# Kernel optimization log

Hardware: AMD Instinct MI355X
Metric: run time of the kernel (lower is better)

Reference implementation:

```python
import jax, jax.numpy as jnp
import numpy as np

IN_FEATURES = 4096
OUT_FEATURES = 4096
RANKS = (1, 16, 16, 1)
M_IN = 16   # in_core_features, 16**3 == 4096
M_OUT = 16  # out_core_features
ORDER = 3


def setup_inputs() -> dict:
    key = jax.random.key(0)
    k_x, k0, k1, k2, kb = jax.random.split(key, 5)
    s = 0.05
    x = jax.random.normal(k_x, (2, 1024, IN_FEATURES), dtype=jnp.float32)
    core0 = jax.random.normal(k0, (RANKS[0], M_IN, M_OUT, RANKS[1]), dtype=jnp.float32) * s
    core1 = jax.random.normal(k1, (RANKS[1], M_IN, M_OUT, RANKS[2]), dtype=jnp.float32) * s
    core2 = jax.random.normal(k2, (RANKS[2], M_IN, M_OUT, RANKS[3]), dtype=jnp.float32) * s
    bound = 1.0 / np.sqrt(IN_FEATURES)
    bias = jax.random.uniform(kb, (OUT_FEATURES,), dtype=jnp.float32,
                              minval=-bound, maxval=bound)
    return {"x": x, "core0": core0, "core1": core1, "core2": core2, "bias": bias}


def reference(x, core0, core1, core2, bias):
    lead_shape = x.shape[:-1]
    pad = M_IN ** ORDER - IN_FEATURES  # 0 here, kept for generality
    xf = x.reshape(-1, IN_FEATURES)
    if pad:
        xf = jnp.pad(xf, ((0, 0), (0, pad)))
    t = xf.reshape(-1, M_IN, M_IN, M_IN)                 # [b, i1, i2, i3]
    # TT core chain contraction (cores: [r_i, i, o, r_{i+1}])
    t = jnp.einsum('bijk,pixq->bjkxq', t, core0)          # sum i1, r0 -> [b, i2, i3, o1, r1]
    t = jnp.einsum('bjkxq,qjyr->bkxyr', t, core1)         # sum i2, r1 -> [b, i3, o1, o2, r2]
    t = jnp.einsum('bkxyr,rkzs->bxyzs', t, core2)         # sum i3, r2 -> [b, o1, o2, o3, 1]
    out = t.reshape(t.shape[0], -1)[:, :OUT_FEATURES]     # truncate padded output dims
    out = out.reshape(*lead_shape, OUT_FEATURES) + bias
    return out
```

## Files before the change

### kernel.cpp

```cpp
#include <hip/hip_runtime.h>
#include <hip/hip_bf16.h>

typedef unsigned short ushort_t;
typedef __attribute__((ext_vector_type(4))) float f32x4;
typedef __attribute__((ext_vector_type(8))) short bf16x8;
typedef __attribute__((ext_vector_type(8))) unsigned short u16x8;

#define M_DIM 2048
#define N_DIM 4096
#define K_DIM 4096
#define BM 256
#define BN 128
#define BK 64
#define NT (K_DIM / BK)

#define MFMA16(a, b, c) __builtin_amdgcn_mfma_f32_16x16x32_bf16((a), (b), (c), 0, 0, 0)

__device__ __forceinline__ unsigned short f2bf(float f) {
  unsigned int u = __float_as_uint(f);
  u += 0x7FFFu + ((u >> 16) & 1u);
  return (unsigned short)(u >> 16);
}

__device__ __forceinline__ void async16(void* l, const void* g) {
  __builtin_amdgcn_global_load_lds(
      (const __attribute__((address_space(1))) void*)g,
      (__attribute__((address_space(3))) void*)l,
      16, 0, 0);
}

__global__ void k_prep(const float* __restrict__ x, ushort_t* __restrict__ o,
                       const float* __restrict__ c0, const float* __restrict__ c1,
                       const float* __restrict__ c2, ushort_t* __restrict__ wt) {
  __shared__ float sc1[16 * 260];
  const int bid = blockIdx.x;
  const int tid = threadIdx.x;
  if (bid < 2048) {
    const int n4 = (M_DIM * K_DIM) / 4;
    for (int i = bid * 256 + tid; i < n4; i += 2048 * 256) {
      float4 v = ((const float4*)x)[i];
      ushort4 r;
      r.x = f2bf(v.x); r.y = f2bf(v.y); r.z = f2bf(v.z); r.w = f2bf(v.w);
      ((ushort4*)o)[i] = r;
    }
  } else {
    const int out = bid - 2048;
    const int o3 = out & 15;
    const int o2 = (out >> 4) & 15;
    const int o1 = out >> 8;

    {
      const int q  = tid >> 4;
      const int i2 = tid & 15;
      const float* src = c1 + q * 4096 + i2 * 256 + o2 * 16;
      float* dst = &sc1[i2 * 260 + q * 16];
      #pragma unroll
      for (int rr = 0; rr < 4; ++rr)
        *(float4*)(dst + rr * 4) = *(const float4*)(src + rr * 4);
    }
    __syncthreads();

    const int i2 = tid & 15;
    const int i1 = tid >> 4;

    float4 a4[4];
    {
      const float* c0p = c0 + (i1 * 16 + o1) * 16;
      #pragma unroll
      for (int rr = 0; rr < 4; ++rr) a4[rr] = *(const float4*)(c0p + rr * 4);
    }

    float t01r[16];
    #pragma unroll
    for (int r = 0; r < 16; ++r) t01r[r] = 0.f;
    #pragma unroll
    for (int q = 0; q < 16; ++q) {
      const float a = a4[q >> 2][q & 3];
      const float* sp = &sc1[i2 * 260 + q * 16];
      #pragma unroll
      for (int rr = 0; rr < 4; ++rr) {
        float4 v = *(const float4*)(sp + rr * 4);
        t01r[rr * 4 + 0] += a * v.x;
        t01r[rr * 4 + 1] += a * v.y;
        t01r[rr * 4 + 2] += a * v.z;
        t01r[rr * 4 + 3] += a * v.w;
      }
    }

    u16x8 lo, hi;
    #pragma unroll
    for (int i3 = 0; i3 < 16; ++i3) {
      const float* c2p = c2 + i3 * 16 + o3;
      float s = 0.f;
      #pragma unroll
      for (int rr = 0; rr < 16; ++rr) s += t01r[rr] * c2p[rr * 256];
      ushort_t v = f2bf(s);
      if (i3 < 8) lo[i3] = v; else hi[i3 - 8] = v;
    }
    u16x8* dst = (u16x8*)(wt + ((size_t)out << 12) + (i1 << 8) + (i2 << 4));
    dst[0] = lo;
    dst[1] = hi;
  }
}

__global__ __launch_bounds__(512, 2) void k_gemm(
    const ushort_t* __restrict__ A,
    const ushort_t* __restrict__ Bt,
    const float* __restrict__ bias,
    float* __restrict__ C)
{
  __shared__ ushort_t lA[3][BM * BK];
  __shared__ ushort_t lB[3][BN * BK];

  const int tid  = threadIdx.x;
  const int lane = tid & 63;
  const int wid  = tid >> 6;
  const int wm   = wid >> 1;
  const int wn   = wid & 1;
  const int fr   = lane & 15;
  const int fg   = lane >> 4;

  const int bid = blockIdx.x;
  const int bm  = bid & 7;
  const int bn  = bid >> 3;

  const int srow = tid >> 3;
  const int scol = ((tid & 7) ^ (srow & 7)) << 3;
  const ushort_t* aSt = A  + (size_t)(bm * BM + srow) * K_DIM + scol;
  const ushort_t* bSt = Bt + (size_t)(bn * BN + srow) * K_DIM + scol;
  const int dE = tid * 8;

#define STAGE_A(kt, s, r_) async16(&lA[s][(r_) * 4096 + dE], \
                                   aSt + (size_t)(kt) * BK + (size_t)(r_) * 64 * K_DIM)
#define STAGE_B(kt, s, r_) async16(&lB[s][(r_) * 4096 + dE], \
                                   bSt + (size_t)(kt) * BK + (size_t)(r_) * 64 * K_DIM)

  const int arowb = wm * 64 + fr;
  const int browb = wn * 64 + fr;
  const int c0 = ( fg      ^ (fr & 7)) << 3;
  const int c1 = ((fg + 4) ^ (fr & 7)) << 3;

  f32x4 acc[4][4];
  #pragma unroll
  for (int m = 0; m < 4; ++m)
    #pragma unroll
    for (int n = 0; n < 4; ++n)
      acc[m][n] = (f32x4){0.f, 0.f, 0.f, 0.f};

  #pragma unroll
  for (int r_ = 0; r_ < 4; ++r_) STAGE_A(0, 0, r_);
  #pragma unroll
  for (int r_ = 0; r_ < 2; ++r_) STAGE_B(0, 0, r_);
  #pragma unroll
  for (int r_ = 0; r_ < 4; ++r_) STAGE_A(1, 1, r_);
  #pragma unroll
  for (int r_ = 0; r_ < 2; ++r_) STAGE_B(1, 1, r_);

  asm volatile("s_waitcnt vmcnt(6)" ::: "memory");
  __builtin_amdgcn_s_barrier();

  int sc = 0, ss = 2;
  for (int t = 0; t < NT; ++t) {
    const bool pre = (t + 2 < NT);
    const ushort_t* pA = &lA[sc][0];
    const ushort_t* pB = &lB[sc][0];

    {
      bf16x8 af[4], bf[4];
      #pragma unroll
      for (int m = 0; m < 4; ++m) af[m] = *(const bf16x8*)(pA + (arowb + m * 16) * 64 + c0);
      #pragma unroll
      for (int n = 0; n < 4; ++n) bf[n] = *(const bf16x8*)(pB + (browb + n * 16) * 64 + c0);
      if (pre) { STAGE_A(t + 2, ss, 0); STAGE_A(t + 2, ss, 1); STAGE_A(t + 2, ss, 2); }
      __builtin_amdgcn_s_barrier();
      __builtin_amdgcn_s_setprio(1);
      #pragma unroll
      for (int m = 0; m < 4; ++m)
        #pragma unroll
        for (int n = 0; n < 4; ++n)
          acc[m][n] = MFMA16(af[m], bf[n], acc[m][n]);
      __builtin_amdgcn_s_setprio(0);
      __builtin_amdgcn_s_barrier();
    }

    {
      bf16x8 af[4], bf[4];
      #pragma unroll
      for (int m = 0; m < 4; ++m) af[m] = *(const bf16x8*)(pA + (arowb + m * 16) * 64 + c1);
      #pragma unroll
      for (int n = 0; n < 4; ++n) bf[n] = *(const bf16x8*)(pB + (browb + n * 16) * 64 + c1);
      if (pre) { STAGE_A(t + 2, ss, 3); STAGE_B(t + 2, ss, 0); STAGE_B(t + 2, ss, 1); }
      __builtin_amdgcn_s_barrier();
      __builtin_amdgcn_s_setprio(1);
      #pragma unroll
      for (int m = 0; m < 4; ++m)
        #pragma unroll
        for (int n = 0; n < 4; ++n)
          acc[m][n] = MFMA16(af[m], bf[n], acc[m][n]);
      __builtin_amdgcn_s_setprio(0);
      if (t + 2 < NT)      asm volatile("s_waitcnt vmcnt(6)" ::: "memory");
      else if (t + 1 < NT) asm volatile("s_waitcnt vmcnt(0)" ::: "memory");
      __builtin_amdgcn_s_barrier();
    }

    sc = (sc == 2) ? 0 : sc + 1;
    ss = (ss == 2) ? 0 : ss + 1;
  }
#undef STAGE_A
#undef STAGE_B

  const size_t row0 = (size_t)bm * BM + wm * 64;
  const int col0 = bn * BN + wn * 64;
  #pragma unroll
  for (int n = 0; n < 4; ++n) {
    const int col = col0 + n * 16 + fr;
    const float bv = bias[col];
    #pragma unroll
    for (int m = 0; m < 4; ++m) {
      const size_t r0 = row0 + m * 16 + fg * 4;
      #pragma unroll
      for (int r = 0; r < 4; ++r)
        C[(r0 + r) * N_DIM + col] = acc[m][n][r] + bv;
    }
  }
}

extern "C" void kernel_launch(void* const* d_in, const int* in_sizes, int n_in,
                              void* d_out, int out_size, void* d_ws, size_t ws_size,
                              hipStream_t stream) {
  const float* x    = (const float*)d_in[0];
  const float* c0   = (const float*)d_in[1];
  const float* c1   = (const float*)d_in[2];
  const float* c2   = (const float*)d_in[3];
  const float* bias = (const float*)d_in[4];
  float* out = (float*)d_out;

  const size_t NEED = (size_t)48 * 1024 * 1024;
  if (ws_size < NEED) return;

  char* ws = (char*)d_ws;
  ushort_t* Abf = (ushort_t*)ws;
  ushort_t* Wt  = (ushort_t*)(ws + (size_t)16 * 1024 * 1024);

  k_prep <<<6144, 256, 0, stream>>>(x, Abf, c0, c1, c2, Wt);
  k_gemm <<<256, 512, 0, stream>>>(Abf, Wt, bias, out);
}
```

Baseline: 106.6 us.

## Add split-K GEMM with 256x256 tiles and bf16 partial reduction kernel

Adds a split-K GEMM path that uses larger 256x256 output tiles with double-buffered LDS and splits K into two halves across blocks. Half 0 writes fp32 partials to the output and half 1 writes bf16 partials to workspace. A separate reduce kernel then adds the partials and the bias. The larger tiles raise data reuse per block, at the cost of an extra kernel, extra memory traffic for the partials, and precision loss from rounding one partial to bf16. This path runs only when the workspace is at least 64 MB; otherwise the old kernel is used.

```diff
diff --git a/kernel.cpp b/kernel.cpp
--- a/kernel.cpp
+++ b/kernel.cpp
@@ -9,10 +9,6 @@
 #define M_DIM 2048
 #define N_DIM 4096
 #define K_DIM 4096
-#define BM 256
-#define BN 128
-#define BK 64
-#define NT (K_DIM / BK)
 
 #define MFMA16(a, b, c) __builtin_amdgcn_mfma_f32_16x16x32_bf16((a), (b), (c), 0, 0, 0)
 
@@ -20,6 +16,9 @@
   unsigned int u = __float_as_uint(f);
   u += 0x7FFFu + ((u >> 16) & 1u);
   return (unsigned short)(u >> 16);
+}
+__device__ __forceinline__ float bf2f(unsigned short u) {
+  return __uint_as_float(((unsigned int)u) << 16);
 }
 
 __device__ __forceinline__ void async16(void* l, const void* g) {
@@ -48,7 +47,6 @@
     const int o3 = out & 15;
     const int o2 = (out >> 4) & 15;
     const int o1 = out >> 8;
-
     {
       const int q  = tid >> 4;
       const int i2 = tid & 15;
@@ -62,14 +60,12 @@
 
     const int i2 = tid & 15;
     const int i1 = tid >> 4;
-
     float4 a4[4];
     {
       const float* c0p = c0 + (i1 * 16 + o1) * 16;
       #pragma unroll
       for (int rr = 0; rr < 4; ++rr) a4[rr] = *(const float4*)(c0p + rr * 4);
     }
-
     float t01r[16];
     #pragma unroll
     for (int r = 0; r < 16; ++r) t01r[r] = 0.f;
@@ -86,7 +82,6 @@
         t01r[rr * 4 + 3] += a * v.w;
       }
     }
-
     u16x8 lo, hi;
     #pragma unroll
     for (int i3 = 0; i3 < 16; ++i3) {
@@ -103,14 +98,160 @@
   }
 }
 
-__global__ __launch_bounds__(512, 2) void k_gemm(
+__global__ __launch_bounds__(512, 1) void k_gemm_sk(
+    const ushort_t* __restrict__ A,
+    const ushort_t* __restrict__ Bt,
+    float* __restrict__ C0,
+    ushort_t* __restrict__ P1b)
+{
+  __shared__ ushort_t lA[2][256 * 64];
+  __shared__ ushort_t lB[2][256 * 64];
+
+  const int tid  = threadIdx.x;
+  const int lane = tid & 63;
+  const int wid  = tid >> 6;
+  const int wm   = wid >> 2;
+  const int wn   = wid & 3;
+  const int fr   = lane & 15;
+  const int fg   = lane >> 4;
+
+  const int bid = blockIdx.x;
+  const int bm  = bid & 7;
+  const int rst = bid >> 3;
+  const int bn  = rst & 15;
+  const int kz  = rst >> 4;
+
+  const int srow = tid >> 3;
+  const int scol = ((tid & 7) ^ (srow & 7)) << 3;
+  const ushort_t* aSt = A  + (size_t)(bm * 256 + srow) * K_DIM + kz * 2048 + scol;
+  const ushort_t* bSt = Bt + (size_t)(bn * 256 + srow) * K_DIM + kz * 2048 + scol;
+  const int dE = tid * 8;
+
+#define SA(kt, s, r4) async16(&lA[s][(r4) * 4096 + dE], \
+                              aSt + (size_t)(kt) * 64 + (size_t)(r4) * 64 * K_DIM)
+#define SB(kt, s, r4) async16(&lB[s][(r4) * 4096 + dE], \
+                              bSt + (size_t)(kt) * 64 + (size_t)(r4) * 64 * K_DIM)
+
+  const int aRow = (wm * 128 + fr) * 64;
+  const int bRow = (wn * 64 + fr) * 64;
+  const int cs0 = ( fg      ^ (fr & 7)) << 3;
+  const int cs1 = ((fg + 4) ^ (fr & 7)) << 3;
+
+  f32x4 acc[8][4];
+  #pragma unroll
+  for (int m = 0; m < 8; ++m)
+    #pragma unroll
+    for (int n = 0; n < 4; ++n)
+      acc[m][n] = (f32x4){0.f, 0.f, 0.f, 0.f};
+
+  SA(0, 0, 0); SA(0, 0, 1); SA(0, 0, 2); SA(0, 0, 3);
+  SB(0, 0, 0); SB(0, 0, 1); SB(0, 0, 2); SB(0, 0, 3);
+  asm volatile("s_waitcnt vmcnt(0)" ::: "memory");
+  __builtin_amdgcn_s_barrier();
+
+  for (int t = 0; t < 32; ++t) {
+    const int s = t & 1;
+    const bool pre = (t + 1 < 32);
+    const ushort_t* pA = &lA[s][0];
+    const ushort_t* pB = &lB[s][0];
+
+    bf16x8 b0[4], b1[4], af[4];
+
+    #pragma unroll
+    for (int n = 0; n < 4; ++n) b0[n] = *(const bf16x8*)(pB + bRow + n * 1024 + cs0);
+    #pragma unroll
+    for (int m = 0; m < 4; ++m) af[m] = *(const bf16x8*)(pA + aRow + m * 1024 + cs0);
+    if (pre) { SA(t + 1, s ^ 1, 0); SA(t + 1, s ^ 1, 1); SA(t + 1, s ^ 1, 2); SA(t + 1, s ^ 1, 3); }
+    __builtin_amdgcn_s_barrier();
+    __builtin_amdgcn_s_setprio(1);
+    #pragma unroll
+    for (int m = 0; m < 4; ++m)
+      #pragma unroll
+      for (int n = 0; n < 4; ++n)
+        acc[m][n] = MFMA16(af[m], b0[n], acc[m][n]);
+    __builtin_amdgcn_s_setprio(0);
+    __builtin_amdgcn_s_barrier();
+
+    #pragma unroll
+    for (int m = 0; m < 4; ++m) af[m] = *(const bf16x8*)(pA + aRow + (4 + m) * 1024 + cs0);
+    if (pre) { SB(t + 1, s ^ 1, 0); SB(t + 1, s ^ 1, 1); SB(t + 1, s ^ 1, 2); SB(t + 1, s ^ 1, 3); }
+    __builtin_amdgcn_s_barrier();
+    __builtin_amdgcn_s_setprio(1);
+    #pragma unroll
+    for (int m = 0; m < 4; ++m)
+      #pragma unroll
+      for (int n = 0; n < 4; ++n)
+        acc[4 + m][n] = MFMA16(af[m], b0[n], acc[4 + m][n]);
+    __builtin_amdgcn_s_setprio(0);
+    __builtin_amdgcn_s_barrier();
+
+    #pragma unroll
+    for (int n = 0; n < 4; ++n) b1[n] = *(const bf16x8*)(pB + bRow + n * 1024 + cs1);
+    #pragma unroll
+    for (int m = 0; m < 4; ++m) af[m] = *(const bf16x8*)(pA + aRow + m * 1024 + cs1);
+    __builtin_amdgcn_s_barrier();
+    __builtin_amdgcn_s_setprio(1);
+    #pragma unroll
+    for (int m = 0; m < 4; ++m)
+      #pragma unroll
+      for (int n = 0; n < 4; ++n)
+        acc[m][n] = MFMA16(af[m], b1[n], acc[m][n]);
+    __builtin_amdgcn_s_setprio(0);
+    __builtin_amdgcn_s_barrier();
+
+    #pragma unroll
+    for (int m = 0; m < 4; ++m) af[m] = *(const bf16x8*)(pA + aRow + (4 + m) * 1024 + cs1);
+    asm volatile("s_waitcnt vmcnt(0)" ::: "memory");
+    __builtin_amdgcn_s_barrier();
+    __builtin_amdgcn_s_setprio(1);
+    #pragma unroll
+    for (int m = 0; m < 4; ++m)
+      #pragma unroll
+      for (int n = 0; n < 4; ++n)
+        acc[4 + m][n] = MFMA16(af[m], b1[n], acc[4 + m][n]);
+    __builtin_amdgcn_s_setprio(0);
+    __builtin_amdgcn_s_barrier();
+  }
+#undef SA
+#undef SB
+
+  const size_t row0 = (size_t)bm * 256 + wm * 128;
+  const int col0 = bn * 256 + wn * 64;
+  if (kz == 0) {
+    #pragma unroll
+    for (int n = 0; n < 4; ++n) {
+      const int col = col0 + n * 16 + fr;
+      #pragma unroll
+      for (int m = 0; m < 8; ++m) {
+        const size_t r0 = row0 + m * 16 + fg * 4;
+        #pragma unroll
+        for (int r = 0; r < 4; ++r)
+          C0[(r0 + r) * N_DIM + col] = acc[m][n][r];
+      }
+    }
+  } else {
+    #pragma unroll
+    for (int n = 0; n < 4; ++n) {
+      const int col = col0 + n * 16 + fr;
+      #pragma unroll
+      for (int m = 0; m < 8; ++m) {
+        const size_t r0 = row0 + m * 16 + fg * 4;
+        #pragma unroll
+        for (int r = 0; r < 4; ++r)
+          P1b[(r0 + r) * N_DIM + col] = f2bf(acc[m][n][r]);
+      }
+    }
+  }
+}
+
+__global__ __launch_bounds__(512, 2) void k_gemm_fb(
     const ushort_t* __restrict__ A,
     const ushort_t* __restrict__ Bt,
     const float* __restrict__ bias,
     float* __restrict__ C)
 {
-  __shared__ ushort_t lA[3][BM * BK];
-  __shared__ ushort_t lB[3][BN * BK];
+  __shared__ ushort_t lA[3][128 * 128];
+  __shared__ ushort_t lB[3][64 * 128];
 
   const int tid  = threadIdx.x;
   const int lane = tid & 63;
@@ -126,14 +267,14 @@
 
   const int srow = tid >> 3;
   const int scol = ((tid & 7) ^ (srow & 7)) << 3;
-  const ushort_t* aSt = A  + (size_t)(bm * BM + srow) * K_DIM + scol;
-  const ushort_t* bSt = Bt + (size_t)(bn * BN + srow) * K_DIM + scol;
+  const ushort_t* aSt = A  + (size_t)(bm * 256 + srow) * K_DIM + scol;
+  const ushort_t* bSt = Bt + (size_t)(bn * 128 + srow) * K_DIM + scol;
   const int dE = tid * 8;
 
 #define STAGE_A(kt, s, r_) async16(&lA[s][(r_) * 4096 + dE], \
-                                   aSt + (size_t)(kt) * BK + (size_t)(r_) * 64 * K_DIM)
+                                   aSt + (size_t)(kt) * 64 + (size_t)(r_) * 64 * K_DIM)
 #define STAGE_B(kt, s, r_) async16(&lB[s][(r_) * 4096 + dE], \
-                                   bSt + (size_t)(kt) * BK + (size_t)(r_) * 64 * K_DIM)
+                                   bSt + (size_t)(kt) * 64 + (size_t)(r_) * 64 * K_DIM)
 
   const int arowb = wm * 64 + fr;
   const int browb = wn * 64 + fr;
@@ -160,11 +301,10 @@
   __builtin_amdgcn_s_barrier();
 
   int sc = 0, ss = 2;
-  for (int t = 0; t < NT; ++t) {
-    const bool pre = (t + 2 < NT);
+  for (int t = 0; t < 64; ++t) {
+    const bool pre = (t + 2 < 64);
     const ushort_t* pA = &lA[sc][0];
     const ushort_t* pB = &lB[sc][0];
-
     {
       bf16x8 af[4], bf[4];
       #pragma unroll
@@ -182,7 +322,6 @@
       __builtin_amdgcn_s_setprio(0);
       __builtin_amdgcn_s_barrier();
     }
-
     {
       bf16x8 af[4], bf[4];
       #pragma unroll
@@ -198,19 +337,18 @@
         for (int n = 0; n < 4; ++n)
           acc[m][n] = MFMA16(af[m], bf[n], acc[m][n]);
       __builtin_amdgcn_s_setprio(0);
-      if (t + 2 < NT)      asm volatile("s_waitcnt vmcnt(6)" ::: "memory");
-      else if (t + 1 < NT) asm volatile("s_waitcnt vmcnt(0)" ::: "memory");
+      if (t + 2 < 64)      asm volatile("s_waitcnt vmcnt(6)" ::: "memory");
+      else if (t + 1 < 64) asm volatile("s_waitcnt vmcnt(0)" ::: "memory");
       __builtin_amdgcn_s_barrier();
     }
-
     sc = (sc == 2) ? 0 : sc + 1;
     ss = (ss == 2) ? 0 : ss + 1;
   }
 #undef STAGE_A
 #undef STAGE_B
 
-  const size_t row0 = (size_t)bm * BM + wm * 64;
-  const int col0 = bn * BN + wn * 64;
+  const size_t row0 = (size_t)bm * 256 + wm * 64;
+  const int col0 = bn * 128 + wn * 64;
   #pragma unroll
   for (int n = 0; n < 4; ++n) {
     const int col = col0 + n * 16 + fr;
@@ -223,6 +361,24 @@
         C[(r0 + r) * N_DIM + col] = acc[m][n][r] + bv;
     }
   }
+}
+
+__global__ void k_reduce(float* __restrict__ out, const ushort_t* __restrict__ p1,
+                         const float* __restrict__ bias) {
+  const int idx = blockIdx.x * 256 + threadIdx.x;
+  const int base = idx * 8;
+  const int col = base & (N_DIM - 1);
+  float4 o0 = *(float4*)(out + base);
+  float4 o1 = *(float4*)(out + base + 4);
+  u16x8 p = *(const u16x8*)(p1 + base);
+  float4 b0 = *(const float4*)(bias + col);
+  float4 b1 = *(const float4*)(bias + col + 4);
+  o0.x += bf2f(p[0]) + b0.x;  o0.y += bf2f(p[1]) + b0.y;
+  o0.z += bf2f(p[2]) + b0.z;  o0.w += bf2f(p[3]) + b0.w;
+  o1.x += bf2f(p[4]) + b1.x;  o1.y += bf2f(p[5]) + b1.y;
+  o1.z += bf2f(p[6]) + b1.z;  o1.w += bf2f(p[7]) + b1.w;
+  *(float4*)(out + base)     = o0;
+  *(float4*)(out + base + 4) = o1;
 }
 
 extern "C" void kernel_launch(void* const* d_in, const int* in_sizes, int n_in,
@@ -235,13 +391,20 @@
   const float* bias = (const float*)d_in[4];
   float* out = (float*)d_out;
 
-  const size_t NEED = (size_t)48 * 1024 * 1024;
-  if (ws_size < NEED) return;
+  const size_t MB = 1024 * 1024;
+  if (ws_size < 48 * MB) return;
 
   char* ws = (char*)d_ws;
   ushort_t* Abf = (ushort_t*)ws;
-  ushort_t* Wt  = (ushort_t*)(ws + (size_t)16 * 1024 * 1024);
-
-  k_prep <<<6144, 256, 0, stream>>>(x, Abf, c0, c1, c2, Wt);
-  k_gemm <<<256, 512, 0, stream>>>(Abf, Wt, bias, out);
-}
+  ushort_t* Wt  = (ushort_t*)(ws + 16 * MB);
+
+  k_prep<<<6144, 256, 0, stream>>>(x, Abf, c0, c1, c2, Wt);
+
+  if (ws_size >= 64 * MB) {
+    ushort_t* P1b = (ushort_t*)(ws + 48 * MB);
+    k_gemm_sk<<<256, 512, 0, stream>>>(Abf, Wt, out, P1b);
+    k_reduce <<<4096, 256, 0, stream>>>(out, P1b, bias);
+  } else {
+    k_gemm_fb<<<256, 512, 0, stream>>>(Abf, Wt, bias, out);
+  }
+}
```

Result: slower. 125.6 us (+17.8%).

## Switch GEMM to split-K with 256x256 tiles and a separate reduce kernel

Applied to the files above, without the earlier changes.

The GEMM now uses 256x256 output tiles and splits K into two halves, so the grid stays at 256 blocks while each block does more MFMA work per loaded byte. The pipeline becomes four-stage with BK=32 and drops the XOR swizzle. The first K-half writes fp32 into the output, the second writes bf16 partials to workspace, and a third kernel adds the partials and bias. This costs an extra launch and extra memory traffic, the bf16 partial rounding adds error, and the unswizzled LDS reads may cause bank conflicts.

```diff
diff --git a/kernel.cpp b/kernel.cpp
--- a/kernel.cpp
+++ b/kernel.cpp
@@ -9,10 +9,8 @@
 #define M_DIM 2048
 #define N_DIM 4096
 #define K_DIM 4096
-#define BM 256
-#define BN 128
-#define BK 64
-#define NT (K_DIM / BK)
+#define BK 32
+#define NT 64
 
 #define MFMA16(a, b, c) __builtin_amdgcn_mfma_f32_16x16x32_bf16((a), (b), (c), 0, 0, 0)
 
@@ -20,6 +18,9 @@
   unsigned int u = __float_as_uint(f);
   u += 0x7FFFu + ((u >> 16) & 1u);
   return (unsigned short)(u >> 16);
+}
+__device__ __forceinline__ float bf2f(unsigned short u) {
+  return __uint_as_float(((unsigned int)u) << 16);
 }
 
 __device__ __forceinline__ void async16(void* l, const void* g) {
@@ -48,7 +49,6 @@
     const int o3 = out & 15;
     const int o2 = (out >> 4) & 15;
     const int o1 = out >> 8;
-
     {
       const int q  = tid >> 4;
       const int i2 = tid & 15;
@@ -62,14 +62,12 @@
 
     const int i2 = tid & 15;
     const int i1 = tid >> 4;
-
     float4 a4[4];
     {
       const float* c0p = c0 + (i1 * 16 + o1) * 16;
       #pragma unroll
       for (int rr = 0; rr < 4; ++rr) a4[rr] = *(const float4*)(c0p + rr * 4);
     }
-
     float t01r[16];
     #pragma unroll
     for (int r = 0; r < 16; ++r) t01r[r] = 0.f;
@@ -86,7 +84,6 @@
         t01r[rr * 4 + 3] += a * v.w;
       }
     }
-
     u16x8 lo, hi;
     #pragma unroll
     for (int i3 = 0; i3 < 16; ++i3) {
@@ -103,126 +100,144 @@
   }
 }
 
-__global__ __launch_bounds__(512, 2) void k_gemm(
+__global__ __launch_bounds__(512, 1) void k_gemm_sk(
     const ushort_t* __restrict__ A,
     const ushort_t* __restrict__ Bt,
-    const float* __restrict__ bias,
-    float* __restrict__ C)
+    float* __restrict__ C0,
+    ushort_t* __restrict__ P1b)
 {
-  __shared__ ushort_t lA[3][BM * BK];
-  __shared__ ushort_t lB[3][BN * BK];
+  __shared__ ushort_t lA[4][256 * BK];
+  __shared__ ushort_t lB[4][256 * BK];
 
   const int tid  = threadIdx.x;
   const int lane = tid & 63;
   const int wid  = tid >> 6;
-  const int wm   = wid >> 1;
-  const int wn   = wid & 1;
+  const int wm   = wid >> 2;
+  const int wn   = wid & 3;
   const int fr   = lane & 15;
   const int fg   = lane >> 4;
 
   const int bid = blockIdx.x;
   const int bm  = bid & 7;
-  const int bn  = bid >> 3;
-
-  const int srow = tid >> 3;
-  const int scol = ((tid & 7) ^ (srow & 7)) << 3;
-  const ushort_t* aSt = A  + (size_t)(bm * BM + srow) * K_DIM + scol;
-  const ushort_t* bSt = Bt + (size_t)(bn * BN + srow) * K_DIM + scol;
+  const int rst = bid >> 3;
+  const int bn  = rst & 15;
+  const int kz  = rst >> 4;
+
+  const int sRow = tid >> 2;
+  const int sQ   = tid & 3;
+  const ushort_t* aSrc = A  + (size_t)(bm * 256 + sRow) * K_DIM + kz * 2048 + sQ * 8;
+  const ushort_t* bSrc = Bt + (size_t)(bn * 256 + sRow) * K_DIM + kz * 2048 + sQ * 8;
   const int dE = tid * 8;
 
-#define STAGE_A(kt, s, r_) async16(&lA[s][(r_) * 4096 + dE], \
-                                   aSt + (size_t)(kt) * BK + (size_t)(r_) * 64 * K_DIM)
-#define STAGE_B(kt, s, r_) async16(&lB[s][(r_) * 4096 + dE], \
-                                   bSt + (size_t)(kt) * BK + (size_t)(r_) * 64 * K_DIM)
-
-  const int arowb = wm * 64 + fr;
-  const int browb = wn * 64 + fr;
-  const int c0 = ( fg      ^ (fr & 7)) << 3;
-  const int c1 = ((fg + 4) ^ (fr & 7)) << 3;
-
-  f32x4 acc[4][4];
+#define SA(kt, s, l) async16(&lA[s][dE + 4096 * (l)], \
+                             aSrc + (size_t)(l) * 128 * K_DIM + (size_t)(kt) * BK)
+#define SB(kt, s, l) async16(&lB[s][dE + 4096 * (l)], \
+                             bSrc + (size_t)(l) * 128 * K_DIM + (size_t)(kt) * BK)
+
+  const int aR0 = (wm * 128 + fr) * BK + fg * 8;
+  const int bR0 = (wn * 64  + fr) * BK + fg * 8;
+
+  f32x4 acc[8][4];
   #pragma unroll
-  for (int m = 0; m < 4; ++m)
+  for (int m = 0; m < 8; ++m)
     #pragma unroll
     for (int n = 0; n < 4; ++n)
       acc[m][n] = (f32x4){0.f, 0.f, 0.f, 0.f};
 
-  #pragma unroll
-  for (int r_ = 0; r_ < 4; ++r_) STAGE_A(0, 0, r_);
-  #pragma unroll
-  for (int r_ = 0; r_ < 2; ++r_) STAGE_B(0, 0, r_);
-  #pragma unroll
-  for (int r_ = 0; r_ < 4; ++r_) STAGE_A(1, 1, r_);
-  #pragma unroll
-  for (int r_ = 0; r_ < 2; ++r_) STAGE_B(1, 1, r_);
-
-  asm volatile("s_waitcnt vmcnt(6)" ::: "memory");
+  SA(0, 0, 0); SA(0, 0, 1); SB(0, 0, 0); SB(0, 0, 1);
+  SA(1, 1, 0); SA(1, 1, 1); SB(1, 1, 0); SB(1, 1, 1);
+  SA(2, 2, 0); SA(2, 2, 1); SB(2, 2, 0); SB(2, 2, 1);
+  asm volatile("s_waitcnt vmcnt(8)" ::: "memory");
   __builtin_amdgcn_s_barrier();
 
-  int sc = 0, ss = 2;
   for (int t = 0; t < NT; ++t) {
-    const bool pre = (t + 2 < NT);
-    const ushort_t* pA = &lA[sc][0];
-    const ushort_t* pB = &lB[sc][0];
-
-    {
-      bf16x8 af[4], bf[4];
-      #pragma unroll
-      for (int m = 0; m < 4; ++m) af[m] = *(const bf16x8*)(pA + (arowb + m * 16) * 64 + c0);
-      #pragma unroll
-      for (int n = 0; n < 4; ++n) bf[n] = *(const bf16x8*)(pB + (browb + n * 16) * 64 + c0);
-      if (pre) { STAGE_A(t + 2, ss, 0); STAGE_A(t + 2, ss, 1); STAGE_A(t + 2, ss, 2); }
-      __builtin_amdgcn_s_barrier();
-      __builtin_amdgcn_s_setprio(1);
-      #pragma unroll
-      for (int m = 0; m < 4; ++m)
+    const int s  = t & 3;
+    const int sp = (t + 3) & 3;
+    const bool pre = (t + 3 < NT);
+    const ushort_t* pA = &lA[s][0];
+    const ushort_t* pB = &lB[s][0];
+
+    bf16x8 bf[4], af[4];
+
+    #pragma unroll
+    for (int n = 0; n < 4; ++n) bf[n] = *(const bf16x8*)(pB + bR0 + n * 16 * BK);
+    #pragma unroll
+    for (int m = 0; m < 4; ++m) af[m] = *(const bf16x8*)(pA + aR0 + m * 16 * BK);
+    if (pre) { SA(t + 3, sp, 0); SA(t + 3, sp, 1); }
+    __builtin_amdgcn_s_barrier();
+    __builtin_amdgcn_s_setprio(1);
+    #pragma unroll
+    for (int m = 0; m < 4; ++m)
+      #pragma unroll
+      for (int n = 0; n < 4; ++n)
+        acc[m][n] = MFMA16(af[m], bf[n], acc[m][n]);
+    __builtin_amdgcn_s_setprio(0);
+    __builtin_amdgcn_s_barrier();
+
+    #pragma unroll
+    for (int m = 0; m < 4; ++m) af[m] = *(const bf16x8*)(pA + aR0 + (64 + m * 16) * BK);
+    if (pre) { SB(t + 3, sp, 0); SB(t + 3, sp, 1); }
+    __builtin_amdgcn_s_barrier();
+    __builtin_amdgcn_s_setprio(1);
+    #pragma unroll
+    for (int m = 0; m < 4; ++m)
+      #pragma unroll
+      for (int n = 0; n < 4; ++n)
+        acc[4 + m][n] = MFMA16(af[m], bf[n], acc[4 + m][n]);
+    __builtin_amdgcn_s_setprio(0);
+    if (t + 3 < NT)      asm volatile("s_waitcnt vmcnt(8)" ::: "memory");
+    else if (t + 2 < NT) asm volatile("s_waitcnt vmcnt(4)" ::: "memory");
+    else if (t + 1 < NT) asm volatile("s_waitcnt vmcnt(0)" ::: "memory");
+    __builtin_amdgcn_s_barrier();
+  }
+#undef SA
+#undef SB
+
+  const size_t row0 = (size_t)bm * 256 + wm * 128;
+  const int col0 = bn * 256 + wn * 64;
+  if (kz == 0) {
+    #pragma unroll
+    for (int n = 0; n < 4; ++n) {
+      const int col = col0 + n * 16 + fr;
+      #pragma unroll
+      for (int m = 0; m < 8; ++m) {
+        const size_t r0 = row0 + m * 16 + fg * 4;
         #pragma unroll
-        for (int n = 0; n < 4; ++n)
-          acc[m][n] = MFMA16(af[m], bf[n], acc[m][n]);
-      __builtin_amdgcn_s_setprio(0);
-      __builtin_amdgcn_s_barrier();
-    }
-
-    {
-      bf16x8 af[4], bf[4];
-      #pragma unroll
-      for (int m = 0; m < 4; ++m) af[m] = *(const bf16x8*)(pA + (arowb + m * 16) * 64 + c1);
-      #pragma unroll
-      for (int n = 0; n < 4; ++n) bf[n] = *(const bf16x8*)(pB + (browb + n * 16) * 64 + c1);
-      if (pre) { STAGE_A(t + 2, ss, 3); STAGE_B(t + 2, ss, 0); STAGE_B(t + 2, ss, 1); }
-      __builtin_amdgcn_s_barrier();
-      __builtin_amdgcn_s_setprio(1);
-      #pragma unroll
-      for (int m = 0; m < 4; ++m)
+        for (int r = 0; r < 4; ++r)
+          C0[(r0 + r) * N_DIM + col] = acc[m][n][r];
+      }
+    }
+  } else {
+    #pragma unroll
+    for (int n = 0; n < 4; ++n) {
+      const int col = col0 + n * 16 + fr;
+      #pragma unroll
+      for (int m = 0; m < 8; ++m) {
+        const size_t r0 = row0 + m * 16 + fg * 4;
         #pragma unroll
-        for (int n = 0; n < 4; ++n)
-          acc[m][n] = MFMA16(af[m], bf[n], acc[m][n]);
-      __builtin_amdgcn_s_setprio(0);
-      if (t + 2 < NT)      asm volatile("s_waitcnt vmcnt(6)" ::: "memory");
-      else if (t + 1 < NT) asm volatile("s_waitcnt vmcnt(0)" ::: "memory");
-      __builtin_amdgcn_s_barrier();
-    }
-
-    sc = (sc == 2) ? 0 : sc + 1;
-    ss = (ss == 2) ? 0 : ss + 1;
+        for (int r = 0; r < 4; ++r)
+          P1b[(r0 + r) * N_DIM + col] = f2bf(acc[m][n][r]);
+      }
+    }
   }
-#undef STAGE_A
-#undef STAGE_B
-
-  const size_t row0 = (size_t)bm * BM + wm * 64;
-  const int col0 = bn * BN + wn * 64;
-  #pragma unroll
-  for (int n = 0; n < 4; ++n) {
-    const int col = col0 + n * 16 + fr;
-    const float bv = bias[col];
-    #pragma unroll
-    for (int m = 0; m < 4; ++m) {
-      const size_t r0 = row0 + m * 16 + fg * 4;
-      #pragma unroll
-      for (int r = 0; r < 4; ++r)
-        C[(r0 + r) * N_DIM + col] = acc[m][n][r] + bv;
-    }
-  }
+}
+
+__global__ void k_reduce(float* __restrict__ out, const ushort_t* __restrict__ p1,
+                         const float* __restrict__ bias) {
+  const int idx = blockIdx.x * 256 + threadIdx.x;
+  const int base = idx * 8;
+  const int col = base & (N_DIM - 1);
+  float4 o0 = *(float4*)(out + base);
+  float4 o1 = *(float4*)(out + base + 4);
+  u16x8 p = *(const u16x8*)(p1 + base);
+  float4 b0 = *(const float4*)(bias + col);
+  float4 b1 = *(const float4*)(bias + col + 4);
+  o0.x += bf2f(p[0]) + b0.x;  o0.y += bf2f(p[1]) + b0.y;
+  o0.z += bf2f(p[2]) + b0.z;  o0.w += bf2f(p[3]) + b0.w;
+  o1.x += bf2f(p[4]) + b1.x;  o1.y += bf2f(p[5]) + b1.y;
+  o1.z += bf2f(p[6]) + b1.z;  o1.w += bf2f(p[7]) + b1.w;
+  *(float4*)(out + base)     = o0;
+  *(float4*)(out + base + 4) = o1;
 }
 
 extern "C" void kernel_launch(void* const* d_in, const int* in_sizes, int n_in,
@@ -235,13 +250,15 @@
   const float* bias = (const float*)d_in[4];
   float* out = (float*)d_out;
 
-  const size_t NEED = (size_t)48 * 1024 * 1024;
-  if (ws_size < NEED) return;
+  const size_t MB = 1024 * 1024;
+  if (ws_size < 64 * MB) return;
 
   char* ws = (char*)d_ws;
   ushort_t* Abf = (ushort_t*)ws;
-  ushort_t* Wt  = (ushort_t*)(ws + (size_t)16 * 1024 * 1024);
-
-  k_prep <<<6144, 256, 0, stream>>>(x, Abf, c0, c1, c2, Wt);
-  k_gemm <<<256, 512, 0, stream>>>(Abf, Wt, bias, out);
-}
+  ushort_t* Wt  = (ushort_t*)(ws + 16 * MB);
+  ushort_t* P1b = (ushort_t*)(ws + 48 * MB);
+
+  k_prep   <<<6144, 256, 0, stream>>>(x, Abf, c0, c1, c2, Wt);
+  k_gemm_sk<<<256, 512, 0, stream>>>(Abf, Wt, out, P1b);
+  k_reduce <<<4096, 256, 0, stream>>>(out, P1b, bias);
+}
```

After: 123.2 us. 1.16x slower.
